# Kernel optimization log

Measured on AMD Instinct MI355X. Metric: run time of the kernel, lower is better.

The kernel has to match this reference:

```python
import jax, jax.numpy as jnp
import numpy as np

N = 100000
E = 1600000
IN = 256
H = 4
D = 32      # n_hidden per head
C = 47      # n_classes
NEG_SLOPE = 0.2


def setup_inputs() -> dict:
    key = jax.random.key(0)
    ks = jax.random.split(key, 16)
    s = 0.1
    inp = {
        "x": jax.random.normal(ks[0], (N, IN), dtype=jnp.float32),
        "src": jax.random.randint(ks[1], (E,), 0, N),
        "dst": jax.random.randint(ks[2], (E,), 0, N),
        # layer 1: IN -> H*D
        "W1": jax.random.normal(ks[3], (IN, H * D), dtype=jnp.float32) * s,
        "al1": jax.random.normal(ks[4], (H, D), dtype=jnp.float32) * s,
        "ar1": jax.random.normal(ks[5], (H, D), dtype=jnp.float32) * s,
        "b1": jnp.zeros((H * D,), dtype=jnp.float32),
        # layer 2: H*D -> H*D
        "W2": jax.random.normal(ks[6], (H * D, H * D), dtype=jnp.float32) * s,
        "al2": jax.random.normal(ks[7], (H, D), dtype=jnp.float32) * s,
        "ar2": jax.random.normal(ks[8], (H, D), dtype=jnp.float32) * s,
        "b2": jnp.zeros((H * D,), dtype=jnp.float32),
        # layer 3: H*D -> H*C
        "W3": jax.random.normal(ks[9], (H * D, H * C), dtype=jnp.float32) * s,
        "al3": jax.random.normal(ks[10], (H, C), dtype=jnp.float32) * s,
        "ar3": jax.random.normal(ks[11], (H, C), dtype=jnp.float32) * s,
        "b3": jnp.zeros((H * C,), dtype=jnp.float32),
    }
    return inp


def gat_conv(h, W, al, ar, b, src, dst, out_dim, activate):
    # h: [N, F_in] -> feat: [N, H, out_dim]
    feat = (h @ W).reshape(N, H, out_dim)
    el = jnp.sum(feat * al[None], axis=-1)          # [N, H]
    er = jnp.sum(feat * ar[None], axis=-1)          # [N, H]
    e = jax.nn.leaky_relu(el[src] + er[dst], NEG_SLOPE)  # [E, H]
    # edge softmax per destination node (segment softmax)
    m = jax.ops.segment_max(e, dst, num_segments=N)      # [N, H]
    ex = jnp.exp(e - m[dst])                             # [E, H]
    den = jax.ops.segment_sum(ex, dst, num_segments=N)   # [N, H]
    alpha = ex / den[dst]                                # [E, H]
    # scatter-weighted aggregation: sum_e alpha_e * feat[src_e]
    out = jax.ops.segment_sum(feat[src] * alpha[:, :, None], dst, num_segments=N)
    out = out + b.reshape(1, H, out_dim)
    return jax.nn.relu(out) if activate else out


def reference(x, src, dst, W1, al1, ar1, b1, W2, al2, ar2, b2, W3, al3, ar3, b3):
    h = gat_conv(x, W1, al1, ar1, b1, src, dst, D, True).reshape(N, H * D)
    h = gat_conv(h, W2, al2, ar2, b2, src, dst, D, True).reshape(N, H * D)
    h = gat_conv(h, W3, al3, ar3, b3, src, dst, C, False)  # [N, H, C]
    h = h.mean(axis=1)                                     # head mean
    return jax.nn.log_softmax(h, axis=-1)
```

## Files before the change

### kernel.cpp

```cpp
#include <hip/hip_runtime.h>
#include <hip/hip_bf16.h>

typedef unsigned short ushort;
typedef unsigned int uint;
typedef __attribute__((ext_vector_type(8))) short short8;
typedef __attribute__((ext_vector_type(4))) float floatx4;
typedef __attribute__((ext_vector_type(2))) float floatx2;

#define NEG_SLOPE 0.2f

__device__ __forceinline__ float bu2f(ushort u) {
  uint t = ((uint)u) << 16;
  return __uint_as_float(t);
}
__device__ __forceinline__ ushort f2bu(float f) {
  __hip_bfloat16 h = __float2bfloat16(f);
  return *(ushort*)&h;
}
__device__ __forceinline__ float lo2f(uint u) { return __uint_as_float(u << 16); }
__device__ __forceinline__ float hi2f(uint u) { return __uint_as_float(u & 0xffff0000u); }
__device__ __forceinline__ float lrelu(float e) { return (e > 0.f) ? e : NEG_SLOPE * e; }
__device__ __forceinline__ float bperm(int byteaddr, float v) {
  return __uint_as_float((uint)__builtin_amdgcn_ds_bpermute(byteaddr, (int)__float_as_uint(v)));
}

__global__ void zero_int_kernel(int* __restrict__ p, int n) {
  int i = blockIdx.x * blockDim.x + threadIdx.x;
  if (i < n) p[i] = 0;
}

__global__ void hist_kernel(const int* __restrict__ dst, int* __restrict__ deg, int E) {
  int e = blockIdx.x * blockDim.x + threadIdx.x;
  if (e < E) atomicAdd(&deg[dst[e]], 1);
}

__global__ void scan1_kernel(const int* __restrict__ deg, int* __restrict__ part,
                             int* __restrict__ bsums, int n) {
  __shared__ int sdata[256];
  int t = threadIdx.x;
  int base = blockIdx.x * 1024;
  int v[4]; int s = 0;
#pragma unroll
  for (int j = 0; j < 4; ++j) {
    int idx = base + t * 4 + j;
    v[j] = (idx < n) ? deg[idx] : 0;
    s += v[j];
  }
  sdata[t] = s;
  __syncthreads();
  for (int off = 1; off < 256; off <<= 1) {
    int x = 0;
    if (t >= off) x = sdata[t - off];
    __syncthreads();
    if (t >= off) sdata[t] += x;
    __syncthreads();
  }
  if (t == 255) bsums[blockIdx.x] = sdata[255];
  int run = (t > 0) ? sdata[t - 1] : 0;
#pragma unroll
  for (int j = 0; j < 4; ++j) {
    int idx = base + t * 4 + j;
    if (idx < n) part[idx] = run;
    run += v[j];
  }
}

__global__ void scan2_kernel(int* __restrict__ bsums, int nb) {
  __shared__ int sdata[256];
  int t = threadIdx.x;
  sdata[t] = (t < nb) ? bsums[t] : 0;
  __syncthreads();
  for (int off = 1; off < 256; off <<= 1) {
    int x = 0;
    if (t >= off) x = sdata[t - off];
    __syncthreads();
    if (t >= off) sdata[t] += x;
    __syncthreads();
  }
  if (t < nb) bsums[t] = (t > 0) ? sdata[t - 1] : 0;
}

__global__ void scan3_kernel(const int* __restrict__ part, const int* __restrict__ bsums,
                             int* __restrict__ rowptr, int* __restrict__ cursor,
                             int n, int Etot) {
  int i = blockIdx.x * blockDim.x + threadIdx.x;
  if (i < n) {
    int v = part[i] + bsums[i >> 10];
    rowptr[i] = v;
    cursor[i] = v;
  }
  if (i == 0) rowptr[n] = Etot;
}

__global__ void scatter_kernel(const int* __restrict__ src, const int* __restrict__ dst,
                               int* __restrict__ cursor, int* __restrict__ csr_src, int E) {
  int e = blockIdx.x * blockDim.x + threadIdx.x;
  if (e < E) {
    int pos = atomicAdd(&cursor[dst[e]], 1);
    csr_src[pos] = src[e];
  }
}

__global__ void splitx_kernel(const float* __restrict__ x, ushort* __restrict__ xhi, int n) {
  int base = (blockIdx.x * blockDim.x + threadIdx.x) * 4;
  if (base >= n) return;
  float4 a = *(const float4*)(x + base);
  float v[4] = {a.x, a.y, a.z, a.w};
  ushort hi[4];
#pragma unroll
  for (int j = 0; j < 4; ++j) hi[j] = f2bu(v[j]);
  uint2 ho;
  ho.x = (uint)hi[0] | ((uint)hi[1] << 16);
  ho.y = (uint)hi[2] | ((uint)hi[3] << 16);
  *(uint2*)(xhi + base) = ho;
}

__global__ void splitW_kernel(const float* __restrict__ W, ushort* __restrict__ WtH,
                              ushort* __restrict__ WtL, int K, int Nc) {
  int idx = blockIdx.x * blockDim.x + threadIdx.x;
  if (idx >= K * Nc) return;
  int n = idx / K, k = idx - n * K;
  float w = W[(size_t)k * Nc + n];
  ushort hi = f2bu(w);
  WtH[idx] = hi;
  WtL[idx] = f2bu(w - bu2f(hi));
}

#define GBM 128
#define GBN 64
#define GBK 32
#define SA 40

__global__ __launch_bounds__(256) void gemm_split_kernel(
    const ushort* __restrict__ A,
    const ushort* __restrict__ Bh, const ushort* __restrict__ Bl,
    ushort* __restrict__ C, int M, int K, int Nc) {
  __shared__ ushort As[GBM * SA];
  __shared__ ushort BsH[GBN * SA];
  __shared__ ushort BsL[GBN * SA];
  int tid = threadIdx.x;
  int lane = tid & 63;
  int wave = tid >> 6;
  int wm = wave & 1, wn = wave >> 1;
  int rowBase = blockIdx.y * GBM;
  int colBase = blockIdx.x * GBN;
  int q = lane >> 4;
  int ln = lane & 15;

  floatx4 acc[4][2] = {};

  for (int k0 = 0; k0 < K; k0 += GBK) {
#pragma unroll
    for (int it = 0; it < 2; ++it) {
      int i = tid + it * 256;
      int r = i >> 2, seg = i & 3;
      int grow = rowBase + r;
      uint4 vh = {0u, 0u, 0u, 0u};
      if (grow < M) {
        size_t off = (size_t)grow * K + k0 + seg * 8;
        vh = *(const uint4*)(A + off);
      }
      *(uint4*)&As[r * SA + seg * 8] = vh;
    }
    {
      int n = tid >> 2, seg = tid & 3;
      int gcol = colBase + n;
      uint4 vh = {0u, 0u, 0u, 0u}, vl = {0u, 0u, 0u, 0u};
      if (gcol < Nc) {
        size_t off = (size_t)gcol * K + k0 + seg * 8;
        vh = *(const uint4*)(Bh + off);
        vl = *(const uint4*)(Bl + off);
      }
      *(uint4*)&BsH[n * SA + seg * 8] = vh;
      *(uint4*)&BsL[n * SA + seg * 8] = vl;
    }
    __syncthreads();
    short8 af[4], bfH[2], bfL[2];
#pragma unroll
    for (int mt = 0; mt < 4; ++mt) {
      int r = (wm * 64 + mt * 16 + ln) * SA + q * 8;
      af[mt] = *(const short8*)&As[r];
    }
#pragma unroll
    for (int nt = 0; nt < 2; ++nt) {
      int r = (wn * 32 + nt * 16 + ln) * SA + q * 8;
      bfH[nt] = *(const short8*)&BsH[r];
      bfL[nt] = *(const short8*)&BsL[r];
    }
#pragma unroll
    for (int mt = 0; mt < 4; ++mt)
#pragma unroll
      for (int nt = 0; nt < 2; ++nt) {
        acc[mt][nt] = __builtin_amdgcn_mfma_f32_16x16x32_bf16(af[mt], bfH[nt], acc[mt][nt], 0, 0, 0);
        acc[mt][nt] = __builtin_amdgcn_mfma_f32_16x16x32_bf16(af[mt], bfL[nt], acc[mt][nt], 0, 0, 0);
      }
    __syncthreads();
  }
#pragma unroll
  for (int mt = 0; mt < 4; ++mt) {
#pragma unroll
    for (int nt = 0; nt < 2; ++nt) {
      int col = colBase + wn * 32 + nt * 16 + ln;
      if (col < Nc) {
#pragma unroll
        for (int r = 0; r < 4; ++r) {
          int row = rowBase + wm * 64 + mt * 16 + q * 4 + r;
          if (row < M) C[(size_t)row * Nc + col] = f2bu(acc[mt][nt][r]);
        }
      }
    }
  }
}

__global__ void elr128_kernel(const ushort* __restrict__ feat, const float* __restrict__ al,
                              const float* __restrict__ ar, float* __restrict__ el,
                              float* __restrict__ er, int N) {
  int g = blockIdx.x * blockDim.x + threadIdx.x;
  if (g >= N * 4) return;
  int n = g >> 2, h = g & 3;
  const uint4* fp = (const uint4*)(feat + (size_t)n * 128 + h * 32);
  const float* alp = al + h * 32;
  const float* arp = ar + h * 32;
  float sl = 0.f, sr = 0.f;
#pragma unroll
  for (int b = 0; b < 4; ++b) {
    uint4 u = fp[b];
    uint w[4] = {u.x, u.y, u.z, u.w};
#pragma unroll
    for (int j = 0; j < 4; ++j) {
      int d = b * 8 + j * 2;
      float f0 = lo2f(w[j]), f1 = hi2f(w[j]);
      sl += f0 * alp[d] + f1 * alp[d + 1];
      sr += f0 * arp[d] + f1 * arp[d + 1];
    }
  }
  el[g] = sl;
  er[g] = sr;
}

__global__ void elr3_kernel(const ushort* __restrict__ feat, const float* __restrict__ al,
                            const float* __restrict__ ar, float* __restrict__ el,
                            float* __restrict__ er, int N) {
  int g = blockIdx.x * blockDim.x + threadIdx.x;
  if (g >= N * 4) return;
  int n = g >> 2, h = g & 3;
  const ushort* fp = feat + (size_t)n * 188 + h * 47;
  float sl = 0.f, sr = 0.f;
  for (int d = 0; d < 47; ++d) {
    float f = bu2f(fp[d]);
    sl += f * al[h * 47 + d];
    sr += f * ar[h * 47 + d];
  }
  el[g] = sl;
  er[g] = sr;
}

__global__ __launch_bounds__(256, 4) void agg128_kernel(
    const int* __restrict__ rowptr, const int* __restrict__ csr_src,
    const ushort* __restrict__ feat, const float* __restrict__ el,
    const float* __restrict__ er, const float* __restrict__ bias,
    ushort* __restrict__ hhi, int N) {
  int lane = threadIdx.x & 63;
  int v = blockIdx.x * 4 + (threadIdx.x >> 6);
  if (v >= N) return;
  float4 er4 = *(const float4*)(er + (size_t)v * 4);
  int r0 = rowptr[v], r1 = rowptr[v + 1];
  int hh = lane & 3;
  float eh = (hh == 0) ? er4.x : (hh == 1) ? er4.y : (hh == 2) ? er4.z : er4.w;
  int hf = lane >> 4;
  int hf4 = hf * 4;
  const uint* fb = (const uint*)feat;
  floatx2 c01 = {0.f, 0.f};
  float densum = 0.f;
  for (int i0 = r0; i0 < r1; i0 += 16) {
    int i = i0 + (lane >> 2);
    int sv = 0;
    float xv = 0.f;
    if (i < r1) {
      sv = csr_src[i];
      xv = __expf(lrelu(el[(size_t)sv * 4 + hh] + eh));
    }
    float ds = xv;
    ds += __shfl_xor(ds, 4);
    ds += __shfl_xor(ds, 8);
    ds += __shfl_xor(ds, 16);
    ds += __shfl_xor(ds, 32);
    densum += ds;
    int cnt = r1 - i0;
    if (cnt > 16) cnt = 16;
    if (cnt == 16) {
#pragma unroll
      for (int j = 0; j < 16; ++j) {
        int s = __builtin_amdgcn_readlane(sv, 4 * j);
        float x = bperm(16 * j + hf4, xv);
        uint u = fb[((size_t)(uint)s << 6) + lane];
        floatx2 f = {lo2f(u), hi2f(u)};
        floatx2 xx = {x, x};
        c01 += xx * f;
      }
    } else {
      for (int j = 0; j < cnt; ++j) {
        int s = __builtin_amdgcn_readlane(sv, 4 * j);
        float x = __shfl(xv, 4 * j + hf);
        uint u = fb[((size_t)(uint)s << 6) + lane];
        floatx2 f = {lo2f(u), hi2f(u)};
        floatx2 xx = {x, x};
        c01 += xx * f;
      }
    }
  }
  float den = __shfl(densum, hf);
  float o0 = (den > 0.f) ? c01.x / den : 0.f;
  float o1 = (den > 0.f) ? c01.y / den : 0.f;
  o0 = fmaxf(o0 + bias[2 * lane], 0.f);
  o1 = fmaxf(o1 + bias[2 * lane + 1], 0.f);
  ushort h0 = f2bu(o0), h1 = f2bu(o1);
  ((uint*)hhi)[(size_t)v * 64 + lane] = (uint)h0 | ((uint)h1 << 16);
}

__global__ __launch_bounds__(256) void agg3_kernel(
    const int* __restrict__ rowptr, const int* __restrict__ csr_src,
    const ushort* __restrict__ feat, const float* __restrict__ el,
    const float* __restrict__ er, const float* __restrict__ bias,
    float* __restrict__ out, int N) {
  __shared__ float svm[4][188];
  int lane = threadIdx.x & 63;
  int w = threadIdx.x >> 6;
  int v = blockIdx.x * 4 + w;
  bool valid = (v < N);
  float4 er4 = {0.f, 0.f, 0.f, 0.f};
  int r0 = 0, r1 = 0;
  if (valid) {
    er4 = *(const float4*)(er + (size_t)v * 4);
    r0 = rowptr[v];
    r1 = rowptr[v + 1];
  }
  int hh = lane & 3;
  float eh = (hh == 0) ? er4.x : (hh == 1) ? er4.y : (hh == 2) ? er4.z : er4.w;
  int fa = 2 * lane, fbi = 2 * lane + 1;
  int fc = 128 + 2 * lane, fd = 129 + 2 * lane;
  bool hasC = (fd < 188);
  int ha = fa / 47, hb = fbi / 47;
  int hc = hasC ? fc / 47 : 3, hd = hasC ? fd / 47 : 3;
  int off2 = hasC ? 64 : 0;
  const uint* fpb = (const uint*)feat;
  float aa = 0.f, ab = 0.f, ac = 0.f, ad = 0.f;
  float densum = 0.f;
  for (int i0 = r0; i0 < r1; i0 += 16) {
    int i = i0 + (lane >> 2);
    int sv = 0;
    float xv = 0.f;
    if (i < r1) {
      sv = csr_src[i];
      xv = __expf(lrelu(el[(size_t)sv * 4 + hh] + eh));
    }
    float ds = xv;
    ds += __shfl_xor(ds, 4);
    ds += __shfl_xor(ds, 8);
    ds += __shfl_xor(ds, 16);
    ds += __shfl_xor(ds, 32);
    densum += ds;
    int cnt = r1 - i0;
    if (cnt > 16) cnt = 16;
#pragma unroll 2
    for (int j = 0; j < cnt; ++j) {
      int s = __builtin_amdgcn_readlane(sv, j * 4);
      float xa = __shfl(xv, j * 4 + ha);
      float xb = __shfl(xv, j * 4 + hb);
      float xc = __shfl(xv, j * 4 + hc);
      float xd = __shfl(xv, j * 4 + hd);
      const uint* fr = fpb + (size_t)(uint)s * 94;
      uint u0 = fr[lane];
      uint u1 = fr[off2 + lane];
      aa = fmaf(xa, lo2f(u0), aa);
      ab = fmaf(xb, hi2f(u0), ab);
      ac = fmaf(xc, lo2f(u1), ac);
      ad = fmaf(xd, hi2f(u1), ad);
    }
  }
  float da = __shfl(densum, ha);
  float db = __shfl(densum, hb);
  float dc = __shfl(densum, hc);
  float dd = __shfl(densum, hd);
  float oa = ((da > 0.f) ? aa / da : 0.f) + bias[fa];
  float ob = ((db > 0.f) ? ab / db : 0.f) + bias[fbi];
  if (valid) {
    svm[w][fa] = oa;
    svm[w][fbi] = ob;
    if (hasC) {
      float oc = ((dc > 0.f) ? ac / dc : 0.f) + bias[fc];
      float od = ((dd > 0.f) ? ad / dd : 0.f) + bias[fd];
      svm[w][fc] = oc;
      svm[w][fd] = od;
    }
  }
  __syncthreads();
  float val = -1e30f;
  if (valid && lane < 47)
    val = 0.25f * (svm[w][lane] + svm[w][47 + lane] + svm[w][94 + lane] + svm[w][141 + lane]);
  float mx = val;
#pragma unroll
  for (int off = 32; off > 0; off >>= 1) mx = fmaxf(mx, __shfl_xor(mx, off));
  float ex = (lane < 47) ? __expf(val - mx) : 0.f;
  float sum = ex;
#pragma unroll
  for (int off = 32; off > 0; off >>= 1) sum += __shfl_xor(sum, off);
  float res = val - mx - logf(sum);
  if (valid && lane < 47) out[(size_t)v * 47 + lane] = res;
}

extern "C" void kernel_launch(void* const* d_in, const int* in_sizes, int n_in,
                              void* d_out, int out_size, void* d_ws, size_t ws_size,
                              hipStream_t stream) {
  const int N = 100000, E = 1600000, IN = 256;
  const int F = 128;
  const int F3 = 188;

  const float* x = (const float*)d_in[0];
  const int* src = (const int*)d_in[1];
  const int* dst = (const int*)d_in[2];
  const float* W1 = (const float*)d_in[3];
  const float* al1 = (const float*)d_in[4];
  const float* ar1 = (const float*)d_in[5];
  const float* b1 = (const float*)d_in[6];
  const float* W2 = (const float*)d_in[7];
  const float* al2 = (const float*)d_in[8];
  const float* ar2 = (const float*)d_in[9];
  const float* b2 = (const float*)d_in[10];
  const float* W3 = (const float*)d_in[11];
  const float* al3 = (const float*)d_in[12];
  const float* ar3 = (const float*)d_in[13];
  const float* b3 = (const float*)d_in[14];

  char* p = (char*)d_ws;
  auto alloc = [&](size_t bytes) -> char* {
    char* r = p;
    p += (bytes + 255) & ~(size_t)255;
    return r;
  };
  ushort* xhi = (ushort*)alloc((size_t)N * IN * sizeof(ushort));
  ushort* feat = (ushort*)alloc((size_t)N * F3 * sizeof(ushort));
  ushort* Wt1h = (ushort*)alloc((size_t)F * IN * sizeof(ushort));
  ushort* Wt1l = (ushort*)alloc((size_t)F * IN * sizeof(ushort));
  ushort* Wt2h = (ushort*)alloc((size_t)F * F * sizeof(ushort));
  ushort* Wt2l = (ushort*)alloc((size_t)F * F * sizeof(ushort));
  ushort* Wt3h = (ushort*)alloc((size_t)F3 * F * sizeof(ushort));
  ushort* Wt3l = (ushort*)alloc((size_t)F3 * F * sizeof(ushort));
  float* el = (float*)alloc((size_t)N * 4 * sizeof(float));
  float* er = (float*)alloc((size_t)N * 4 * sizeof(float));
  int* deg = (int*)alloc((size_t)N * sizeof(int));
  int* part = (int*)alloc((size_t)N * sizeof(int));
  int* bsums = (int*)alloc(256 * sizeof(int));
  int* rowptr = (int*)alloc((size_t)(N + 1) * sizeof(int));
  int* cursor = (int*)alloc((size_t)N * sizeof(int));
  int* csr_src = (int*)alloc((size_t)E * sizeof(int));

  ushort* hhi = xhi;

  zero_int_kernel<<<(N + 255) / 256, 256, 0, stream>>>(deg, N);
  hist_kernel<<<(E + 255) / 256, 256, 0, stream>>>(dst, deg, E);
  int nb = (N + 1023) / 1024;
  scan1_kernel<<<nb, 256, 0, stream>>>(deg, part, bsums, N);
  scan2_kernel<<<1, 256, 0, stream>>>(bsums, nb);
  scan3_kernel<<<(N + 255) / 256, 256, 0, stream>>>(part, bsums, rowptr, cursor, N, E);
  scatter_kernel<<<(E + 255) / 256, 256, 0, stream>>>(src, dst, cursor, csr_src, E);

  splitx_kernel<<<(N * IN / 4 + 255) / 256, 256, 0, stream>>>(x, xhi, N * IN);
  splitW_kernel<<<(IN * F + 255) / 256, 256, 0, stream>>>(W1, Wt1h, Wt1l, IN, F);
  splitW_kernel<<<(F * F + 255) / 256, 256, 0, stream>>>(W2, Wt2h, Wt2l, F, F);
  splitW_kernel<<<(F * F3 + 255) / 256, 256, 0, stream>>>(W3, Wt3h, Wt3l, F, F3);

  int rowBlocks = (N + GBM - 1) / GBM;
  int nodeBlocks = (N + 3) / 4;

  gemm_split_kernel<<<dim3(F / GBN, rowBlocks), 256, 0, stream>>>(
      xhi, Wt1h, Wt1l, feat, N, IN, F);
  elr128_kernel<<<(N * 4 + 255) / 256, 256, 0, stream>>>(feat, al1, ar1, el, er, N);
  agg128_kernel<<<nodeBlocks, 256, 0, stream>>>(rowptr, csr_src, feat, el, er, b1, hhi, N);

  gemm_split_kernel<<<dim3(F / GBN, rowBlocks), 256, 0, stream>>>(
      hhi, Wt2h, Wt2l, feat, N, F, F);
  elr128_kernel<<<(N * 4 + 255) / 256, 256, 0, stream>>>(feat, al2, ar2, el, er, N);
  agg128_kernel<<<nodeBlocks, 256, 0, stream>>>(rowptr, csr_src, feat, el, er, b2, hhi, N);

  gemm_split_kernel<<<dim3((F3 + GBN - 1) / GBN, rowBlocks), 256, 0, stream>>>(
      hhi, Wt3h, Wt3l, feat, N, F, F3);
  elr3_kernel<<<(N * 4 + 255) / 256, 256, 0, stream>>>(feat, al3, ar3, el, er, N);
  agg3_kernel<<<nodeBlocks, 256, 0, stream>>>(rowptr, csr_src, feat, el, er, b3,
                                              (float*)d_out, N);
}
```

Baseline: 850.1 us.

## Pad layer-3 features to 48 per head for uniform head-aligned aggregation

Layer-3 weights are transposed into a padded 192-column layout (48 per head, last column zero), so feature rows are 96 words and each head starts at an aligned offset. The aggregation kernel then gives each 16-lane group a single head, needing one shuffle for the attention weight per edge instead of four, and replacing divisions with a reciprocal multiply. The cost is about 2% more feature bytes per gathered row, plus idle lanes on the second load.

Measured after the change: 834.2 us. No clear change (-1.9%).

```diff
diff --git a/kernel.cpp b/kernel.cpp
--- a/kernel.cpp
+++ b/kernel.cpp
@@ -121,6 +121,18 @@
   if (idx >= K * Nc) return;
   int n = idx / K, k = idx - n * K;
   float w = W[(size_t)k * Nc + n];
+  ushort hi = f2bu(w);
+  WtH[idx] = hi;
+  WtL[idx] = f2bu(w - bu2f(hi));
+}
+
+__global__ void splitW3pad_kernel(const float* __restrict__ W, ushort* __restrict__ WtH,
+                                  ushort* __restrict__ WtL, int K) {
+  int idx = blockIdx.x * blockDim.x + threadIdx.x;
+  if (idx >= K * 192) return;
+  int n = idx / K, k = idx - n * K;
+  int h = n / 48, d = n - h * 48;
+  float w = (d < 47) ? W[(size_t)k * 188 + h * 47 + d] : 0.f;
   ushort hi = f2bu(w);
   WtH[idx] = hi;
   WtL[idx] = f2bu(w - bu2f(hi));
@@ -244,7 +256,7 @@
   int g = blockIdx.x * blockDim.x + threadIdx.x;
   if (g >= N * 4) return;
   int n = g >> 2, h = g & 3;
-  const ushort* fp = feat + (size_t)n * 188 + h * 47;
+  const ushort* fp = feat + (size_t)n * 192 + h * 48;
   float sl = 0.f, sr = 0.f;
   for (int d = 0; d < 47; ++d) {
     float f = bu2f(fp[d]);
@@ -323,7 +335,7 @@
     const ushort* __restrict__ feat, const float* __restrict__ el,
     const float* __restrict__ er, const float* __restrict__ bias,
     float* __restrict__ out, int N) {
-  __shared__ float svm[4][188];
+  __shared__ float svm[4][192];
   int lane = threadIdx.x & 63;
   int w = threadIdx.x >> 6;
   int v = blockIdx.x * 4 + w;
@@ -337,12 +349,12 @@
   }
   int hh = lane & 3;
   float eh = (hh == 0) ? er4.x : (hh == 1) ? er4.y : (hh == 2) ? er4.z : er4.w;
-  int fa = 2 * lane, fbi = 2 * lane + 1;
-  int fc = 128 + 2 * lane, fd = 129 + 2 * lane;
-  bool hasC = (fd < 188);
-  int ha = fa / 47, hb = fbi / 47;
-  int hc = hasC ? fc / 47 : 3, hd = hasC ? fd / 47 : 3;
-  int off2 = hasC ? 64 : 0;
+  int h = lane >> 4;
+  int k = lane & 15;
+  bool hasU1 = (k < 8);
+  float c1 = hasU1 ? 1.f : 0.f;
+  int o0 = h * 24 + k;
+  int o1 = h * 24 + 16 + (k & 7);
   const uint* fpb = (const uint*)feat;
   float aa = 0.f, ab = 0.f, ac = 0.f, ad = 0.f;
   float densum = 0.f;
@@ -365,39 +377,41 @@
 #pragma unroll 2
     for (int j = 0; j < cnt; ++j) {
       int s = __builtin_amdgcn_readlane(sv, j * 4);
-      float xa = __shfl(xv, j * 4 + ha);
-      float xb = __shfl(xv, j * 4 + hb);
-      float xc = __shfl(xv, j * 4 + hc);
-      float xd = __shfl(xv, j * 4 + hd);
-      const uint* fr = fpb + (size_t)(uint)s * 94;
-      uint u0 = fr[lane];
-      uint u1 = fr[off2 + lane];
-      aa = fmaf(xa, lo2f(u0), aa);
-      ab = fmaf(xb, hi2f(u0), ab);
-      ac = fmaf(xc, lo2f(u1), ac);
-      ad = fmaf(xd, hi2f(u1), ad);
-    }
-  }
-  float da = __shfl(densum, ha);
-  float db = __shfl(densum, hb);
-  float dc = __shfl(densum, hc);
-  float dd = __shfl(densum, hd);
-  float oa = ((da > 0.f) ? aa / da : 0.f) + bias[fa];
-  float ob = ((db > 0.f) ? ab / db : 0.f) + bias[fbi];
+      float x = __shfl(xv, j * 4 + h);
+      float x1 = x * c1;
+      const uint* fr = fpb + (size_t)(uint)s * 96;
+      uint u0 = fr[o0];
+      uint u1 = fr[o1];
+      aa = fmaf(x, lo2f(u0), aa);
+      ab = fmaf(x, hi2f(u0), ab);
+      ac = fmaf(x1, lo2f(u1), ac);
+      ad = fmaf(x1, hi2f(u1), ad);
+    }
+  }
+  float dh = __shfl(densum, h);
+  float rd = (dh > 0.f) ? 1.f / dh : 0.f;
+  int f0 = h * 48 + 2 * k, f1 = f0 + 1;
+  int d2 = 32 + 2 * (k & 7), d3 = d2 + 1;
+  int f2 = h * 48 + d2, f3 = h * 48 + d3;
+  int b0 = h * 47 + 2 * k, b1 = b0 + 1;
+  int b2 = h * 47 + d2;
+  int b3i = h * 47 + ((d3 < 47) ? d3 : 46);
+  float oa = aa * rd + bias[b0];
+  float ob = ab * rd + bias[b1];
   if (valid) {
-    svm[w][fa] = oa;
-    svm[w][fbi] = ob;
-    if (hasC) {
-      float oc = ((dc > 0.f) ? ac / dc : 0.f) + bias[fc];
-      float od = ((dd > 0.f) ? ad / dd : 0.f) + bias[fd];
-      svm[w][fc] = oc;
-      svm[w][fd] = od;
+    svm[w][f0] = oa;
+    svm[w][f1] = ob;
+    if (hasU1) {
+      float oc = ac * rd + bias[b2];
+      float od = ad * rd + bias[b3i];
+      svm[w][f2] = oc;
+      svm[w][f3] = od;
     }
   }
   __syncthreads();
   float val = -1e30f;
   if (valid && lane < 47)
-    val = 0.25f * (svm[w][lane] + svm[w][47 + lane] + svm[w][94 + lane] + svm[w][141 + lane]);
+    val = 0.25f * (svm[w][lane] + svm[w][48 + lane] + svm[w][96 + lane] + svm[w][144 + lane]);
   float mx = val;
 #pragma unroll
   for (int off = 32; off > 0; off >>= 1) mx = fmaxf(mx, __shfl_xor(mx, off));
@@ -414,7 +428,7 @@
                               hipStream_t stream) {
   const int N = 100000, E = 1600000, IN = 256;
   const int F = 128;
-  const int F3 = 188;
+  const int F3P = 192;
 
   const float* x = (const float*)d_in[0];
   const int* src = (const int*)d_in[1];
@@ -439,13 +453,13 @@
     return r;
   };
   ushort* xhi = (ushort*)alloc((size_t)N * IN * sizeof(ushort));
-  ushort* feat = (ushort*)alloc((size_t)N * F3 * sizeof(ushort));
+  ushort* feat = (ushort*)alloc((size_t)N * F3P * sizeof(ushort));
   ushort* Wt1h = (ushort*)alloc((size_t)F * IN * sizeof(ushort));
   ushort* Wt1l = (ushort*)alloc((size_t)F * IN * sizeof(ushort));
   ushort* Wt2h = (ushort*)alloc((size_t)F * F * sizeof(ushort));
   ushort* Wt2l = (ushort*)alloc((size_t)F * F * sizeof(ushort));
-  ushort* Wt3h = (ushort*)alloc((size_t)F3 * F * sizeof(ushort));
-  ushort* Wt3l = (ushort*)alloc((size_t)F3 * F * sizeof(ushort));
+  ushort* Wt3h = (ushort*)alloc((size_t)F3P * F * sizeof(ushort));
+  ushort* Wt3l = (ushort*)alloc((size_t)F3P * F * sizeof(ushort));
   float* el = (float*)alloc((size_t)N * 4 * sizeof(float));
   float* er = (float*)alloc((size_t)N * 4 * sizeof(float));
   int* deg = (int*)alloc((size_t)N * sizeof(int));
@@ -468,7 +482,7 @@
   splitx_kernel<<<(N * IN / 4 + 255) / 256, 256, 0, stream>>>(x, xhi, N * IN);
   splitW_kernel<<<(IN * F + 255) / 256, 256, 0, stream>>>(W1, Wt1h, Wt1l, IN, F);
   splitW_kernel<<<(F * F + 255) / 256, 256, 0, stream>>>(W2, Wt2h, Wt2l, F, F);
-  splitW_kernel<<<(F * F3 + 255) / 256, 256, 0, stream>>>(W3, Wt3h, Wt3l, F, F3);
+  splitW3pad_kernel<<<(F * F3P + 255) / 256, 256, 0, stream>>>(W3, Wt3h, Wt3l, F);
 
   int rowBlocks = (N + GBM - 1) / GBM;
   int nodeBlocks = (N + 3) / 4;
@@ -483,8 +497,8 @@
   elr128_kernel<<<(N * 4 + 255) / 256, 256, 0, stream>>>(feat, al2, ar2, el, er, N);
   agg128_kernel<<<nodeBlocks, 256, 0, stream>>>(rowptr, csr_src, feat, el, er, b2, hhi, N);
 
-  gemm_split_kernel<<<dim3((F3 + GBN - 1) / GBN, rowBlocks), 256, 0, stream>>>(
-      hhi, Wt3h, Wt3l, feat, N, F, F3);
+  gemm_split_kernel<<<dim3(F3P / GBN, rowBlocks), 256, 0, stream>>>(
+      hhi, Wt3h, Wt3l, feat, N, F, F3P);
   elr3_kernel<<<(N * 4 + 255) / 256, 256, 0, stream>>>(feat, al3, ar3, el, er, N);
   agg3_kernel<<<nodeBlocks, 256, 0, stream>>>(rowptr, csr_src, feat, el, er, b3,
                                               (float*)d_out, N);
```
